# Kernel tuning notes

Measured on AMD Instinct MI355X. Metric: run time of the kernel, lower is better.

## Reference

```python
import jax, jax.numpy as jnp
import numpy as np
from jax import lax

SAMPLES = 1024  # number of farthest points to select (init arg `samples`)
BIG = 1e10      # stand-in for +inf so min-distance init works in any float dtype


def setup_inputs() -> dict:
    key = jax.random.key(0)
    points = jax.random.normal(key, (32, 131072, 3), dtype=jnp.float32)  # B x N x 3
    return {"points": points}


def reference(points) -> jnp.ndarray:
    """Farthest point sampling: greedily pick SAMPLES points maximizing
    min-distance to the already-selected set. Returns B x SAMPLES x 3."""
    B, N, _ = points.shape
    init_idx = jnp.zeros((B,), dtype=jnp.int32)          # start from point 0 per batch
    init_dist = jnp.full((B, N), BIG, dtype=points.dtype)  # running min sq-dist to selected set

    def step(carry, _):
        dist, last_idx = carry
        last_pt = jnp.take_along_axis(points, last_idx[:, None, None], axis=1)
        d = jnp.sum((points - last_pt) ** 2, axis=-1)     # B x N squared distances
        dist = jnp.minimum(dist, d)                        # update min-dist to selected set
        next_idx = jnp.argmax(dist, axis=-1).astype(jnp.int32)
        return (dist, next_idx), last_idx                  # emit the index we just used

    (_, _), idxs = lax.scan(step, (init_dist, init_idx), None, length=SAMPLES)
    idxs = idxs.T                                          # B x SAMPLES
    sampled = jnp.take_along_axis(points, idxs[..., None], axis=1)  # B x SAMPLES x 3
    return sampled
```

## Files before the change

kernel.cpp:

```cpp
#include <hip/hip_runtime.h>
#include <stdint.h>


#define NB        32
#define NPTS      131072
#define NSAMP     1024
#define CHUNKS    8
#define THREADS   512
#define PPT       32
#define CHUNK_PTS 16384
#define BIGF      1e10f
#define SEQ_MASK  0x7FFFull


__global__ __launch_bounds__(THREADS, 2)
void fps_kernel(const float* __restrict__ pts,
                float* __restrict__ out,
                unsigned long long* __restrict__ keys)
{
    #pragma clang fp contract(off)

    const int b = blockIdx.x & (NB - 1);
    const int c = blockIdx.x >> 5;
    const int t = threadIdx.x;

    __shared__ unsigned long long wkey[THREADS / 64];
    __shared__ float bc_x, bc_y, bc_z;

    const float* bpts = pts + (size_t)b * NPTS * 3;

    float x[PPT], y[PPT], z[PPT], dist[PPT];
    #pragma unroll
    for (int i = 0; i < PPT; ++i) {
        const int n = c * CHUNK_PTS + i * THREADS + t;
        x[i] = bpts[3 * n + 0];
        y[i] = bpts[3 * n + 1];
        z[i] = bpts[3 * n + 2];
        dist[i] = BIGF;
    }

    float px = bpts[0], py = bpts[1], pz = bpts[2];
    if (c == 0 && t == 0) {
        out[(size_t)b * NSAMP * 3 + 0] = px;
        out[(size_t)b * NSAMP * 3 + 1] = py;
        out[(size_t)b * NSAMP * 3 + 2] = pz;
    }

    for (int s = 1; s < NSAMP; ++s) {
        float bv = -1.0f;
        int   bi = 0;
        #pragma unroll
        for (int i = 0; i < PPT; ++i) {
            const float dx = x[i] - px;
            const float dy = y[i] - py;
            const float dz = z[i] - pz;
            float d = dx * dx;
            d = d + dy * dy;
            d = d + dz * dz;
            const float nd = fminf(dist[i], d);
            dist[i] = nd;
            if (nd > bv) { bv = nd; bi = c * CHUNK_PTS + i * THREADS + t; }
        }

        #pragma unroll
        for (int off = 32; off > 0; off >>= 1) {
            const float ov = __shfl_xor(bv, off);
            const int   oi = __shfl_xor(bi, off);
            if (ov > bv || (ov == bv && oi < bi)) { bv = ov; bi = oi; }
        }
        if ((t & 63) == 0) {
            wkey[t >> 6] = ((unsigned long long)__float_as_uint(bv) << 32)
                         | ((unsigned long long)(NPTS - 1 - bi) << 15)
                         | (unsigned long long)s;
        }
        __syncthreads();

        if (t < 64) {
            unsigned long long k = (t < THREADS / 64) ? wkey[t] : 0ull;
            #pragma unroll
            for (int off = 1; off < 8; off <<= 1) {
                const unsigned long long ok = __shfl_xor(k, off);
                if (ok > k) k = ok;
            }
            unsigned long long* kslot = keys + ((size_t)(s & 1) * NB + b) * CHUNKS;
            if (t == 0)
                __hip_atomic_store(&kslot[c], k, __ATOMIC_RELAXED, __HIP_MEMORY_SCOPE_AGENT);
            __atomic_signal_fence(__ATOMIC_SEQ_CST);

            unsigned long long pk = 0;
            if (t < CHUNKS) {
                do {
                    pk = __hip_atomic_load(&kslot[t], __ATOMIC_RELAXED, __HIP_MEMORY_SCOPE_AGENT);
                } while ((pk & SEQ_MASK) != (unsigned long long)s);
            }
            #pragma unroll
            for (int off = 1; off < 8; off <<= 1) {
                const unsigned long long ok = __shfl_xor(pk, off);
                if (ok > pk) pk = ok;
            }
            if (t == 0) {
                const int widx = (NPTS - 1) - (int)((pk >> 15) & 0x1FFFF);
                const float wx = bpts[3 * (size_t)widx + 0];
                const float wy = bpts[3 * (size_t)widx + 1];
                const float wz = bpts[3 * (size_t)widx + 2];
                bc_x = wx; bc_y = wy; bc_z = wz;
                if (c == 0) {
                    const size_t o = ((size_t)b * NSAMP + s) * 3;
                    out[o + 0] = wx; out[o + 1] = wy; out[o + 2] = wz;
                }
            }
        }
        __syncthreads();
        px = bc_x; py = bc_y; pz = bc_z;
    }
}

extern "C" void kernel_launch(void* const* d_in, const int* in_sizes, int n_in,
                              void* d_out, int out_size, void* d_ws, size_t ws_size,
                              hipStream_t stream)
{
    const float* pts = (const float*)d_in[0];
    float* out = (float*)d_out;

    unsigned long long* keys = (unsigned long long*)d_ws;

    fps_kernel<<<dim3(NB * CHUNKS), dim3(THREADS), 0, stream>>>(pts, out, keys);
}
```

Measured before the change: 3.171 ms.

## Double chunk count per batch and let every wave poll global keys directly

The per-batch work is split across 16 blocks instead of 8, halving the points each thread holds, and launch bounds are raised to allow 4 blocks per CU. The second block-wide barrier and the shared-memory broadcast of the winner are removed: every wave now spins on the global key slots itself, reduces them and loads the winning point. The goal is to cut the per-sample critical path of compute plus intra-block synchronisation. The cost is more blocks to gather at each step, more polling traffic on the key slots, and reliance on all 512 blocks being co-resident to avoid deadlock.

```diff
diff --git a/kernel.cpp b/kernel.cpp
--- a/kernel.cpp
+++ b/kernel.cpp
@@ -5,27 +5,29 @@
 #define NB        32
 #define NPTS      131072
 #define NSAMP     1024
-#define CHUNKS    8
+#define CHUNKS    16
 #define THREADS   512
-#define PPT       32
-#define CHUNK_PTS 16384
+#define WAVES     (THREADS / 64)
+#define PPT       (NPTS / (CHUNKS * THREADS))
+#define CHUNK_PTS (NPTS / CHUNKS)
 #define BIGF      1e10f
 #define SEQ_MASK  0x7FFFull
 
 
-__global__ __launch_bounds__(THREADS, 2)
+__global__ __launch_bounds__(THREADS, 4)
 void fps_kernel(const float* __restrict__ pts,
                 float* __restrict__ out,
                 unsigned long long* __restrict__ keys)
 {
     #pragma clang fp contract(off)
 
-    const int b = blockIdx.x & (NB - 1);
-    const int c = blockIdx.x >> 5;
-    const int t = threadIdx.x;
+    const int b    = blockIdx.x & (NB - 1);
+    const int c    = blockIdx.x >> 5;
+    const int t    = threadIdx.x;
+    const int w    = t >> 6;
+    const int lane = t & 63;
 
-    __shared__ unsigned long long wkey[THREADS / 64];
-    __shared__ float bc_x, bc_y, bc_z;
+    __shared__ unsigned long long wkey[WAVES];
 
     const float* bpts = pts + (size_t)b * NPTS * 3;
 
@@ -68,50 +70,49 @@
             const int   oi = __shfl_xor(bi, off);
             if (ov > bv || (ov == bv && oi < bi)) { bv = ov; bi = oi; }
         }
-        if ((t & 63) == 0) {
-            wkey[t >> 6] = ((unsigned long long)__float_as_uint(bv) << 32)
-                         | ((unsigned long long)(NPTS - 1 - bi) << 15)
-                         | (unsigned long long)s;
+        if (lane == 0) {
+            wkey[w] = ((unsigned long long)__float_as_uint(bv) << 32)
+                    | ((unsigned long long)(NPTS - 1 - bi) << 15)
+                    | (unsigned long long)s;
         }
         __syncthreads();
 
-        if (t < 64) {
-            unsigned long long k = (t < THREADS / 64) ? wkey[t] : 0ull;
+        unsigned long long* kslot = keys + ((size_t)(s & 1) * NB + b) * CHUNKS;
+
+        if (w == 0) {
+            unsigned long long k = (lane < WAVES) ? wkey[lane] : 0ull;
             #pragma unroll
-            for (int off = 1; off < 8; off <<= 1) {
+            for (int off = 1; off < WAVES; off <<= 1) {
                 const unsigned long long ok = __shfl_xor(k, off);
                 if (ok > k) k = ok;
             }
-            unsigned long long* kslot = keys + ((size_t)(s & 1) * NB + b) * CHUNKS;
-            if (t == 0)
+            if (lane == 0)
                 __hip_atomic_store(&kslot[c], k, __ATOMIC_RELAXED, __HIP_MEMORY_SCOPE_AGENT);
-            __atomic_signal_fence(__ATOMIC_SEQ_CST);
+        }
+        __atomic_signal_fence(__ATOMIC_SEQ_CST);
 
-            unsigned long long pk = 0;
-            if (t < CHUNKS) {
-                do {
-                    pk = __hip_atomic_load(&kslot[t], __ATOMIC_RELAXED, __HIP_MEMORY_SCOPE_AGENT);
-                } while ((pk & SEQ_MASK) != (unsigned long long)s);
-            }
-            #pragma unroll
-            for (int off = 1; off < 8; off <<= 1) {
-                const unsigned long long ok = __shfl_xor(pk, off);
-                if (ok > pk) pk = ok;
-            }
-            if (t == 0) {
-                const int widx = (NPTS - 1) - (int)((pk >> 15) & 0x1FFFF);
-                const float wx = bpts[3 * (size_t)widx + 0];
-                const float wy = bpts[3 * (size_t)widx + 1];
-                const float wz = bpts[3 * (size_t)widx + 2];
-                bc_x = wx; bc_y = wy; bc_z = wz;
-                if (c == 0) {
-                    const size_t o = ((size_t)b * NSAMP + s) * 3;
-                    out[o + 0] = wx; out[o + 1] = wy; out[o + 2] = wz;
-                }
-            }
+        unsigned long long pk = 0;
+        if (lane < CHUNKS) {
+            do {
+                pk = __hip_atomic_load(&kslot[lane], __ATOMIC_RELAXED, __HIP_MEMORY_SCOPE_AGENT);
+            } while ((pk & SEQ_MASK) != (unsigned long long)s);
         }
-        __syncthreads();
-        px = bc_x; py = bc_y; pz = bc_z;
+        #pragma unroll
+        for (int off = 1; off < CHUNKS; off <<= 1) {
+            const unsigned long long ok = __shfl_xor(pk, off);
+            if (ok > pk) pk = ok;
+        }
+        pk = __shfl(pk, 0);
+
+        const int widx = (NPTS - 1) - (int)((pk >> 15) & 0x1FFFF);
+        px = bpts[3 * (size_t)widx + 0];
+        py = bpts[3 * (size_t)widx + 1];
+        pz = bpts[3 * (size_t)widx + 2];
+
+        if (c == 0 && t == 0) {
+            const size_t o = ((size_t)b * NSAMP + s) * 3;
+            out[o + 0] = px; out[o + 1] = py; out[o + 2] = pz;
+        }
     }
 }
 
```

After: 4.162 ms. +31.3%, slower.
